# Optimization experiments

Measured on AMD Instinct MI355X. Metric: run time of the kernel, lower is better.

Reference implementation:

```python
import jax, jax.numpy as jnp
import numpy as np

D_MODEL = 1024
NUM_HEADS = 16


def setup_inputs() -> dict:
    key = jax.random.key(0)
    ks = jax.random.split(key, 5)
    B, S, D = 2, 2048, D_MODEL
    x = jax.random.normal(ks[0], (B, S, D), dtype=jnp.float32)
    # nn.Linear(d_model, d_model, bias=False) weights, shape [out, in]
    scale = 1.0 / np.sqrt(D)
    Wq = jax.random.normal(ks[1], (D, D), dtype=jnp.float32) * scale
    Wk = jax.random.normal(ks[2], (D, D), dtype=jnp.float32) * scale
    Wv = jax.random.normal(ks[3], (D, D), dtype=jnp.float32) * scale
    Wo = jax.random.normal(ks[4], (D, D), dtype=jnp.float32) * scale
    return {"x": x, "Wq": Wq, "Wk": Wk, "Wv": Wv, "Wo": Wo}


def reference(x, Wq, Wk, Wv, Wo):
    B, S, D = x.shape
    H = NUM_HEADS
    dh = D // H
    # projections: x @ W.T (Linear without bias)
    q = (x @ Wq.T).reshape(B, S, H, dh).transpose(0, 2, 1, 3)  # [B,H,S,dh]
    k = (x @ Wk.T).reshape(B, S, H, dh).transpose(0, 2, 1, 3)
    v = (x @ Wv.T).reshape(B, S, H, dh).transpose(0, 2, 1, 3)
    scores = jnp.einsum("bhqd,bhkd->bhqk", q, k) / jnp.sqrt(jnp.float32(dh))
    # causal mask: positions j > i get -inf before softmax
    causal = jnp.triu(jnp.ones((S, S), dtype=bool), k=1)
    scores = jnp.where(causal, -jnp.inf, scores)
    attn = jax.nn.softmax(scores, axis=-1)  # [B,H,S,S]
    out = jnp.einsum("bhqk,bhkd->bhqd", attn, v)  # [B,H,S,dh]
    out = out.transpose(0, 2, 1, 3).reshape(B, S, D)
    return out @ Wo.T
```

## Files before the change

kernel.cpp:

```cpp
#include <hip/hip_runtime.h>

typedef __attribute__((ext_vector_type(8))) __bf16 bf16x8;
typedef __attribute__((ext_vector_type(4))) __bf16 bf16x4;
typedef __attribute__((ext_vector_type(2))) __bf16 bf16x2;
typedef __attribute__((ext_vector_type(4))) float f32x4;
typedef __attribute__((ext_vector_type(16))) float f32x16;
typedef __attribute__((ext_vector_type(4))) unsigned uint4v;

static constexpr int S = 2048;
static constexpr int D = 1024;
static constexpr int BATCH = 2;
static constexpr int M_ROWS = BATCH * S;

#define GLOAD_LDS16(gp, lp)                                                        \
  __builtin_amdgcn_global_load_lds((const __attribute__((address_space(1))) void*)(gp), \
                                   (__attribute__((address_space(3))) void*)(lp), 16, 0, 0)

__global__ __launch_bounds__(256) void cast_all(const float* __restrict__ x,
                                                const float* __restrict__ w0, const float* __restrict__ w1,
                                                const float* __restrict__ w2, const float* __restrict__ w3,
                                                __bf16* __restrict__ xo,
                                                __bf16* __restrict__ o0, __bf16* __restrict__ o1,
                                                __bf16* __restrict__ o2, __bf16* __restrict__ o3) {
  const int bid = blockIdx.x;
  const float* in;
  __bf16* out;
  int base;
  if (bid < 4096) {
    in = x; out = xo; base = bid;
  } else {
    const int wi = (bid - 4096) >> 10;
    in = wi == 0 ? w0 : wi == 1 ? w1 : wi == 2 ? w2 : w3;
    out = wi == 0 ? o0 : wi == 1 ? o1 : wi == 2 ? o2 : o3;
    base = (bid - 4096) & 1023;
  }
  int i = (base * 256 + threadIdx.x) * 4;
  *reinterpret_cast<bf16x4*>(out + i) =
      __builtin_convertvector(*reinterpret_cast<const f32x4*>(in + i), bf16x4);
}

template <typename OutT>
__device__ __forceinline__ void gemm_core(const __bf16* __restrict__ A,
                                          const __bf16* __restrict__ Bm,
                                          OutT* __restrict__ C, int m0, int n0, int K, int ldc,
                                          __bf16* At, __bf16* Bt) {
  const int tid = threadIdx.x;
  const int w = tid >> 6, l = tid & 63;
  const int wr = w >> 1, wc = w & 1;
  const int ln = l & 15, gr = l >> 4;

  const int srow = w * 32 + (l >> 3);
  const int scol = ((l & 7) ^ (l >> 3)) * 8;
  const size_t aoff = (size_t)(m0 + srow) * K + scol;
  const size_t boff = (size_t)(n0 + srow) * K + scol;
  __bf16* lA = At + w * 2048;
  __bf16* lB = Bt + w * 2048;

  f32x4 acc[4][4] = {};

  for (int k0 = 0; k0 < K; k0 += 64) {
    __syncthreads();
#pragma unroll
    for (int j = 0; j < 4; j++) {
      GLOAD_LDS16(A + aoff + (size_t)(j * 8) * K + k0, lA + j * 512);
      GLOAD_LDS16(Bm + boff + (size_t)(j * 8) * K + k0, lB + j * 512);
    }
    __syncthreads();

#pragma unroll
    for (int ks = 0; ks < 2; ks++) {
      bf16x8 af[4], bfr[4];
#pragma unroll
      for (int mi = 0; mi < 4; mi++) {
        const int R = wr * 64 + mi * 16 + ln;
        af[mi] = *reinterpret_cast<const bf16x8*>(
            &At[R * 64 + (((ks * 4 + gr) ^ (R & 7)) * 8)]);
      }
#pragma unroll
      for (int ni = 0; ni < 4; ni++) {
        const int R = wc * 64 + ni * 16 + ln;
        bfr[ni] = *reinterpret_cast<const bf16x8*>(
            &Bt[R * 64 + (((ks * 4 + gr) ^ (R & 7)) * 8)]);
      }
#pragma unroll
      for (int mi = 0; mi < 4; mi++)
#pragma unroll
        for (int ni = 0; ni < 4; ni++)
          acc[mi][ni] = __builtin_amdgcn_mfma_f32_16x16x32_bf16(af[mi], bfr[ni], acc[mi][ni], 0, 0, 0);
    }
  }

#pragma unroll
  for (int mi = 0; mi < 4; mi++)
#pragma unroll
    for (int ni = 0; ni < 4; ni++)
#pragma unroll
      for (int r = 0; r < 4; r++) {
        int row = m0 + wr * 64 + mi * 16 + gr * 4 + r;
        int col = n0 + wc * 64 + ni * 16 + ln;
        float v = acc[mi][ni][r];
        if constexpr (__is_same(OutT, float))
          C[(size_t)row * ldc + col] = v;
        else
          C[(size_t)row * ldc + col] = (__bf16)v;
      }
}

__global__ __launch_bounds__(256) void qkv_gemm(const __bf16* __restrict__ xb,
                                                const __bf16* __restrict__ wq,
                                                const __bf16* __restrict__ wk,
                                                const __bf16* __restrict__ wv,
                                                __bf16* __restrict__ q, __bf16* __restrict__ k,
                                                __bf16* __restrict__ vt) {
  __shared__ __bf16 At[128 * 64];
  __shared__ __bf16 Bt[128 * 64];
  const int id = (blockIdx.x & 7) * 96 + (blockIdx.x >> 3);
  const __bf16 *A, *B;
  __bf16* C;
  int m0, n0, ldc;
  if (id < 512) {
    A = xb;
    B = (id < 256) ? wq : wk;
    C = (id < 256) ? q : k;
    int t = id & 255;
    m0 = (t >> 3) * 128;
    n0 = (t & 7) * 128;
    ldc = 1024;
  } else {
    int t = id - 512;
    A = wv;
    B = xb;
    C = vt;
    m0 = (t & 7) * 128;
    n0 = (t >> 3) * 128;
    ldc = 4096;
  }
  gemm_core<__bf16>(A, B, C, m0, n0, 1024, ldc, At, Bt);
}

__global__ __launch_bounds__(256) void wo_gemm(const __bf16* __restrict__ ob,
                                               const __bf16* __restrict__ wo,
                                               float* __restrict__ out) {
  __shared__ __bf16 At[128 * 64];
  __shared__ __bf16 Bt[128 * 64];
  const int wg = (blockIdx.x & 7) * 32 + (blockIdx.x >> 3);
  gemm_core<float>(ob, wo, out, (wg >> 3) * 128, (wg & 7) * 128, 1024, 1024, At, Bt);
}

__global__ __launch_bounds__(512, 2) void attn_kernel(const __bf16* __restrict__ Qb,
                                                      const __bf16* __restrict__ Kb,
                                                      const __bf16* __restrict__ VTb,
                                                      __bf16* __restrict__ Ob) {
  __shared__ __bf16 mo[8][64][32];
  __shared__ float mml[8][64][2];

  const int lin = blockIdx.x;
  const int wid = ((lin & 7) << 5) | (lin >> 3);
  const int bh = wid >> 3;
  const int ib = wid & 7;
  const int b = bh >> 4, h = bh & 15;

  const int tid = threadIdx.x;
  const int w = tid >> 6, l = tid & 63;
  const int q31 = l & 31, hi = l >> 5;
  const int pp = w & 3, hf = w >> 2;

  const int j = ib * 4 + pp;
  const int q0A = j * 32, q0B = (63 - j) * 32;
  const int nA = j + 1, nB = 64 - j;
  const int nhA = (nA + 1) >> 1, nhB = (nB + 1) >> 1;
  const int sA = hf ? nhA : 0, cA = hf ? nA - nhA : nhA;
  const int sB = hf ? nhB : 0, cB = hf ? nB - nhB : nhB;

  const __bf16* Qp = Qb + (size_t)b * S * D + h * 64;
  const __bf16* Kp = Kb + (size_t)b * S * D + h * 64;
  const __bf16* Vt = VTb + (size_t)(h * 64) * M_ROWS + b * S;

  const float SCALE2 = 0.125f * 1.44269504f;
  const float NEG = -1e30f;
  const float THR_RAW = 8.0f / SCALE2;

  bf16x8 qfA[4], qfB[4];
#pragma unroll
  for (int ds = 0; ds < 4; ds++) {
    qfA[ds] = *reinterpret_cast<const bf16x8*>(Qp + (size_t)(q0A + q31) * D + ds * 16 + hi * 8);
    qfB[ds] = *reinterpret_cast<const bf16x8*>(Qp + (size_t)(q0B + q31) * D + ds * 16 + hi * 8);
  }

  f32x16 oaccA[2] = {}, oaccB[2] = {};
  float mrA = NEG, lsA = 0.f, mrB = NEG, lsB = 0.f;

  auto loadK = [&](bf16x8 (&dst)[4], int kk) {
#pragma unroll
    for (int ds = 0; ds < 4; ds++)
      dst[ds] = *reinterpret_cast<const bf16x8*>(
          Kp + (size_t)(kk + q31) * D + ds * 16 + hi * 8);
  };
  auto loadV = [&](bf16x8 (&dst)[2][2], int kk) {
#pragma unroll
    for (int d0 = 0; d0 < 2; d0++)
#pragma unroll
      for (int ks = 0; ks < 2; ks++)
        dst[d0][ks] = *reinterpret_cast<const bf16x8*>(
            Vt + (size_t)(d0 * 32 + q31) * M_ROWS + kk + ks * 16 + hi * 8);
  };
  auto qk1 = [&](f32x16& st, bf16x8 (&kf)[4], bf16x8 (&qf)[4]) {
    f32x16 z = {};
#pragma unroll
    for (int ds = 0; ds < 4; ds++)
      z = __builtin_amdgcn_mfma_f32_32x32x16_bf16(kf[ds], qf[ds], z, 0, 0, 0);
    st = z;
  };
  auto pack2 = [](float x, float y) -> unsigned {
    bf16x2 p;
    p[0] = (__bf16)x;
    p[1] = (__bf16)y;
    return __builtin_bit_cast(unsigned, p);
  };
  auto maskmax = [&](f32x16& st, bool tail, float (&pv)[16]) -> float {
#pragma unroll
    for (int r = 0; r < 16; r++) {
      float v = st[r];
      if (tail) {
        int keyidx = (r & 3) + 8 * (r >> 2) + 4 * hi;
        v = (keyidx <= q31) ? v : NEG;
      }
      pv[r] = v;
    }
    float t8[8], t4[4];
#pragma unroll
    for (int ii = 0; ii < 8; ii++) t8[ii] = fmaxf(pv[ii], pv[ii + 8]);
#pragma unroll
    for (int ii = 0; ii < 4; ii++) t4[ii] = fmaxf(t8[ii], t8[ii + 4]);
    float tm = fmaxf(fmaxf(t4[0], t4[1]), fmaxf(t4[2], t4[3]));
    return fmaxf(tm, __shfl_xor(tm, 32));
  };
  auto rescale = [&](float& mr, float& ls, f32x16& o0, f32x16& o1, float tm) {
    float nm = fmaxf(mr, tm);
    float a = __builtin_exp2f((mr - nm) * SCALE2);
    mr = nm;
    ls *= a;
#pragma unroll
    for (int r = 0; r < 16; r++) o0[r] *= a;
#pragma unroll
    for (int r = 0; r < 16; r++) o1[r] *= a;
  };
  auto expsum = [&](float (&pv)[16], float mr, float& ls, unsigned (&dw)[8]) {
    const float mrs = mr * SCALE2;
#pragma unroll
    for (int r = 0; r < 16; r++)
      pv[r] = __builtin_exp2f(__builtin_fmaf(pv[r], SCALE2, -mrs));
    float s8[8], s4[4];
#pragma unroll
    for (int ii = 0; ii < 8; ii++) s8[ii] = pv[ii] + pv[ii + 8];
#pragma unroll
    for (int ii = 0; ii < 4; ii++) s4[ii] = s8[ii] + s8[ii + 4];
    float ps = (s4[0] + s4[1]) + (s4[2] + s4[3]);
    ps += __shfl_xor(ps, 32);
    ls += ps;
#pragma unroll
    for (int bb = 0; bb < 4; bb++) {
      dw[2 * bb] = pack2(pv[4 * bb], pv[4 * bb + 1]);
      dw[2 * bb + 1] = pack2(pv[4 * bb + 2], pv[4 * bb + 3]);
    }
  };
  auto pvmma = [&](unsigned (&dw)[8], bf16x8 (&vf)[2][2], f32x16& o0, f32x16& o1) {
#pragma unroll
    for (int ks = 0; ks < 2; ks++) {
      unsigned s0v = hi ? dw[4 * ks + 0] : dw[4 * ks + 2];
      unsigned s1v = hi ? dw[4 * ks + 1] : dw[4 * ks + 3];
      unsigned r0 = (unsigned)__shfl_xor((int)s0v, 32);
      unsigned r1 = (unsigned)__shfl_xor((int)s1v, 32);
      uint4v uv;
      uv.x = hi ? r0 : dw[4 * ks + 0];
      uv.y = hi ? r1 : dw[4 * ks + 1];
      uv.z = hi ? dw[4 * ks + 2] : r0;
      uv.w = hi ? dw[4 * ks + 3] : r1;
      bf16x8 pb = __builtin_bit_cast(bf16x8, uv);
      o0 = __builtin_amdgcn_mfma_f32_32x32x16_bf16(vf[0][ks], pb, o0, 0, 0, 0);
      o1 = __builtin_amdgcn_mfma_f32_32x32x16_bf16(vf[1][ks], pb, o1, 0, 0, 0);
    }
  };

  bf16x8 kfA[4], kfB[4], vfA[2][2], vfB[2][2];
  f32x16 stA, stB;

  if (cA > 0) {
    loadK(kfA, sA * 32);
    loadV(vfA, sA * 32);
  }
  loadK(kfB, sB * 32);
  loadV(vfB, sB * 32);

  for (int i2 = 0; i2 < cA; i2++) {
    __builtin_amdgcn_s_setprio(1);
    qk1(stA, kfA, qfA);
    qk1(stB, kfB, qfB);
    __builtin_amdgcn_s_setprio(0);
    if (i2 + 1 < cA) loadK(kfA, (sA + i2 + 1) * 32);
    if (i2 + 1 < cB) loadK(kfB, (sB + i2 + 1) * 32);

    float pvA[16], pvB[16];
    float tmA = maskmax(stA, sA + i2 == nA - 1, pvA);
    float tmB = maskmax(stB, sB + i2 == nB - 1, pvB);
    if (!__all((tmA - mrA <= THR_RAW) && (tmB - mrB <= THR_RAW))) {
      rescale(mrA, lsA, oaccA[0], oaccA[1], tmA);
      rescale(mrB, lsB, oaccB[0], oaccB[1], tmB);
    }
    unsigned dwA[8], dwB[8];
    expsum(pvA, mrA, lsA, dwA);
    expsum(pvB, mrB, lsB, dwB);
    __builtin_amdgcn_s_setprio(1);
    pvmma(dwA, vfA, oaccA[0], oaccA[1]);
    pvmma(dwB, vfB, oaccB[0], oaccB[1]);
    __builtin_amdgcn_s_setprio(0);
    if (i2 + 1 < cA) loadV(vfA, (sA + i2 + 1) * 32);
    if (i2 + 1 < cB) loadV(vfB, (sB + i2 + 1) * 32);
  }
  for (int i2 = cA; i2 < cB; i2++) {
    __builtin_amdgcn_s_setprio(1);
    qk1(stB, kfB, qfB);
    __builtin_amdgcn_s_setprio(0);
    if (i2 + 1 < cB) loadK(kfB, (sB + i2 + 1) * 32);
    float pvB[16];
    float tmB = maskmax(stB, sB + i2 == nB - 1, pvB);
    if (!__all(tmB - mrB <= THR_RAW)) rescale(mrB, lsB, oaccB[0], oaccB[1], tmB);
    unsigned dwB[8];
    expsum(pvB, mrB, lsB, dwB);
    __builtin_amdgcn_s_setprio(1);
    pvmma(dwB, vfB, oaccB[0], oaccB[1]);
    __builtin_amdgcn_s_setprio(0);
    if (i2 + 1 < cB) loadV(vfB, (sB + i2 + 1) * 32);
  }

  if (hf == 1) {
#pragma unroll
    for (int d0 = 0; d0 < 2; d0++) {
      bf16x8 pkA, pkB;
#pragma unroll
      for (int rr = 0; rr < 8; rr++) {
        pkA[rr] = (__bf16)oaccA[d0][rr];
        pkB[rr] = (__bf16)oaccB[d0][rr];
      }
      *reinterpret_cast<bf16x8*>(&mo[2 * pp + 0][l][d0 * 16]) = pkA;
      *reinterpret_cast<bf16x8*>(&mo[2 * pp + 1][l][d0 * 16]) = pkB;
      bf16x8 pkA2, pkB2;
#pragma unroll
      for (int rr = 0; rr < 8; rr++) {
        pkA2[rr] = (__bf16)oaccA[d0][8 + rr];
        pkB2[rr] = (__bf16)oaccB[d0][8 + rr];
      }
      *reinterpret_cast<bf16x8*>(&mo[2 * pp + 0][l][d0 * 16 + 8]) = pkA2;
      *reinterpret_cast<bf16x8*>(&mo[2 * pp + 1][l][d0 * 16 + 8]) = pkB2;
    }
    mml[2 * pp + 0][l][0] = mrA;
    mml[2 * pp + 0][l][1] = lsA;
    mml[2 * pp + 1][l][0] = mrB;
    mml[2 * pp + 1][l][1] = lsB;
  }
  __syncthreads();
  if (hf == 0) {
#pragma unroll
    for (int cc = 0; cc < 2; cc++) {
      const int slot = 2 * pp + cc;
      const int q0 = cc ? q0B : q0A;
      f32x16* oacc = cc ? oaccB : oaccA;
      float mr = cc ? mrB : mrA;
      float ls = cc ? lsB : lsA;
      float mr1 = mml[slot][l][0], ls1 = mml[slot][l][1];
      float mc = fmaxf(mr, mr1);
      float a0 = __builtin_exp2f((mr - mc) * SCALE2);
      float a1 = __builtin_exp2f((mr1 - mc) * SCALE2);
      float inv = 1.0f / (ls * a0 + ls1 * a1);
      float f0 = a0 * inv, f1 = a1 * inv;
      size_t row = (size_t)(b * S + q0 + q31);
#pragma unroll
      for (int d0 = 0; d0 < 2; d0++)
#pragma unroll
        for (int bb = 0; bb < 4; bb++) {
          bf16x4 ov;
#pragma unroll
          for (int rr = 0; rr < 4; rr++) {
            float part = (float)mo[slot][l][d0 * 16 + 4 * bb + rr];
            ov[rr] = (__bf16)(oacc[d0][4 * bb + rr] * f0 + part * f1);
          }
          *reinterpret_cast<bf16x4*>(Ob + row * D + h * 64 + d0 * 32 + 8 * bb + 4 * hi) = ov;
        }
    }
  }
}

extern "C" void kernel_launch(void* const* d_in, const int* in_sizes, int n_in,
                              void* d_out, int out_size, void* d_ws, size_t ws_size,
                              hipStream_t stream) {
  const float* x = (const float*)d_in[0];
  const float* Wq = (const float*)d_in[1];
  const float* Wk = (const float*)d_in[2];
  const float* Wv = (const float*)d_in[3];
  const float* Wo = (const float*)d_in[4];
  float* out = (float*)d_out;

  char* ws = (char*)d_ws;
  const size_t MB = 1024 * 1024;
  __bf16* xb = (__bf16*)(ws + 0 * MB);
  __bf16* qb = (__bf16*)(ws + 8 * MB);
  __bf16* kb = (__bf16*)(ws + 16 * MB);
  __bf16* vtb = (__bf16*)(ws + 24 * MB);
  __bf16* ob = (__bf16*)(ws + 32 * MB);
  __bf16* wqb = (__bf16*)(ws + 40 * MB);
  __bf16* wkb = (__bf16*)(ws + 42 * MB);
  __bf16* wvb = (__bf16*)(ws + 44 * MB);
  __bf16* wob = (__bf16*)(ws + 46 * MB);

  cast_all<<<8192, 256, 0, stream>>>(x, Wq, Wk, Wv, Wo, xb, wqb, wkb, wvb, wob);

  qkv_gemm<<<768, 256, 0, stream>>>(xb, wqb, wkb, wvb, qb, kb, vtb);

  attn_kernel<<<256, 512, 0, stream>>>(qb, kb, vtb, ob);

  wo_gemm<<<256, 256, 0, stream>>>(ob, wob, out);
}
```

Baseline: 135.0 us.

## Software-pipeline QK^T one tile ahead of softmax and PV in attention loop

```diff
diff --git a/kernel.cpp b/kernel.cpp
--- a/kernel.cpp
+++ b/kernel.cpp
@@ -283,7 +283,7 @@
   };
 
   bf16x8 kfA[4], kfB[4], vfA[2][2], vfB[2][2];
-  f32x16 stA, stB;
+  f32x16 stA0, stA1, stB0, stB1;
 
   if (cA > 0) {
     loadK(kfA, sA * 32);
@@ -291,46 +291,55 @@
   }
   loadK(kfB, sB * 32);
   loadV(vfB, sB * 32);
-
-  for (int i2 = 0; i2 < cA; i2++) {
+  if (cA > 0) qk1(stA0, kfA, qfA);
+  qk1(stB0, kfB, qfB);
+  if (cA > 1) loadK(kfA, (sA + 1) * 32);
+  if (cB > 1) loadK(kfB, (sB + 1) * 32);
+
+  auto body = [&](f32x16& sAc, f32x16& sAn, f32x16& sBc, f32x16& sBn, int i2) {
+    const bool a_now = i2 < cA;
+    const bool a_nxt = i2 + 1 < cA;
+    const bool b_nxt = i2 + 1 < cB;
     __builtin_amdgcn_s_setprio(1);
-    qk1(stA, kfA, qfA);
-    qk1(stB, kfB, qfB);
+    if (a_nxt) qk1(sAn, kfA, qfA);
+    if (b_nxt) qk1(sBn, kfB, qfB);
     __builtin_amdgcn_s_setprio(0);
-    if (i2 + 1 < cA) loadK(kfA, (sA + i2 + 1) * 32);
-    if (i2 + 1 < cB) loadK(kfB, (sB + i2 + 1) * 32);
+    if (i2 + 2 < cA) loadK(kfA, (sA + i2 + 2) * 32);
+    if (i2 + 2 < cB) loadK(kfB, (sB + i2 + 2) * 32);
 
     float pvA[16], pvB[16];
-    float tmA = maskmax(stA, sA + i2 == nA - 1, pvA);
-    float tmB = maskmax(stB, sB + i2 == nB - 1, pvB);
-    if (!__all((tmA - mrA <= THR_RAW) && (tmB - mrB <= THR_RAW))) {
-      rescale(mrA, lsA, oaccA[0], oaccA[1], tmA);
-      rescale(mrB, lsB, oaccB[0], oaccB[1], tmB);
-    }
-    unsigned dwA[8], dwB[8];
-    expsum(pvA, mrA, lsA, dwA);
-    expsum(pvB, mrB, lsB, dwB);
-    __builtin_amdgcn_s_setprio(1);
-    pvmma(dwA, vfA, oaccA[0], oaccA[1]);
-    pvmma(dwB, vfB, oaccB[0], oaccB[1]);
-    __builtin_amdgcn_s_setprio(0);
-    if (i2 + 1 < cA) loadV(vfA, (sA + i2 + 1) * 32);
-    if (i2 + 1 < cB) loadV(vfB, (sB + i2 + 1) * 32);
-  }
-  for (int i2 = cA; i2 < cB; i2++) {
-    __builtin_amdgcn_s_setprio(1);
-    qk1(stB, kfB, qfB);
-    __builtin_amdgcn_s_setprio(0);
-    if (i2 + 1 < cB) loadK(kfB, (sB + i2 + 1) * 32);
-    float pvB[16];
-    float tmB = maskmax(stB, sB + i2 == nB - 1, pvB);
-    if (!__all(tmB - mrB <= THR_RAW)) rescale(mrB, lsB, oaccB[0], oaccB[1], tmB);
-    unsigned dwB[8];
-    expsum(pvB, mrB, lsB, dwB);
-    __builtin_amdgcn_s_setprio(1);
-    pvmma(dwB, vfB, oaccB[0], oaccB[1]);
-    __builtin_amdgcn_s_setprio(0);
-    if (i2 + 1 < cB) loadV(vfB, (sB + i2 + 1) * 32);
+    float tmB = maskmax(sBc, sB + i2 == nB - 1, pvB);
+    if (a_now) {
+      float tmA = maskmax(sAc, sA + i2 == nA - 1, pvA);
+      if (!__all((tmA - mrA <= THR_RAW) && (tmB - mrB <= THR_RAW))) {
+        rescale(mrA, lsA, oaccA[0], oaccA[1], tmA);
+        rescale(mrB, lsB, oaccB[0], oaccB[1], tmB);
+      }
+      unsigned dwA[8], dwB[8];
+      expsum(pvA, mrA, lsA, dwA);
+      expsum(pvB, mrB, lsB, dwB);
+      __builtin_amdgcn_s_setprio(1);
+      pvmma(dwA, vfA, oaccA[0], oaccA[1]);
+      pvmma(dwB, vfB, oaccB[0], oaccB[1]);
+      __builtin_amdgcn_s_setprio(0);
+    } else {
+      if (!__all(tmB - mrB <= THR_RAW)) rescale(mrB, lsB, oaccB[0], oaccB[1], tmB);
+      unsigned dwB[8];
+      expsum(pvB, mrB, lsB, dwB);
+      __builtin_amdgcn_s_setprio(1);
+      pvmma(dwB, vfB, oaccB[0], oaccB[1]);
+      __builtin_amdgcn_s_setprio(0);
+    }
+    if (a_nxt) loadV(vfA, (sA + i2 + 1) * 32);
+    if (b_nxt) loadV(vfB, (sB + i2 + 1) * 32);
+  };
+
+  int i2 = 0;
+  for (;;) {
+    body(stA0, stA1, stB0, stB1, i2);
+    if (++i2 >= cB) break;
+    body(stA1, stA0, stB1, stB0, i2);
+    if (++i2 >= cB) break;
   }
 
   if (hf == 1) {
```

After: 173.0 us. 1.28x slower.
